# Optimization experiments

Hardware: AMD Instinct MI355X
Metric: run time of the kernel (lower is better)

The kernel has to match this reference:

```python
import jax, jax.numpy as jnp
import numpy as np

HEAD_DIM = 16

def setup_inputs() -> dict:
    key = jax.random.key(0)
    ks = jax.random.split(key, 9)
    dim = 256
    B, H, W = 8, 32, 32
    x  = jax.random.normal(ks[0], (B, H, W, dim), jnp.float32)
    # Conv2d weights in OIHW layout (torch convention), small init
    w3 = jax.random.normal(ks[1], (dim, dim, 1, 1), jnp.float32) * 0.05
    b3 = jax.random.normal(ks[2], (dim,), jnp.float32) * 0.01
    w5 = jax.random.normal(ks[3], (dim, dim, 3, 3), jnp.float32) * 0.02
    b5 = jax.random.normal(ks[4], (dim,), jnp.float32) * 0.01
    w7 = jax.random.normal(ks[5], (dim, dim, 5, 5), jnp.float32) * 0.01
    b7 = jax.random.normal(ks[6], (dim,), jnp.float32) * 0.01
    # nn.Linear weight: (out_features=dim, in_features=attention_dim=dim), no bias
    wp = jax.random.normal(ks[7], (dim, dim), jnp.float32) * 0.05
    return {"x": x, "w3": w3, "b3": b3, "w5": w5, "b5": b5, "w7": w7, "b7": b7, "wp": wp}

def _conv2d_same(x_nchw, w_oihw, b):
    y = jax.lax.conv_general_dilated(
        x_nchw, w_oihw, window_strides=(1, 1), padding='SAME',
        dimension_numbers=('NCHW', 'OIHW', 'NCHW'))
    return y + b[None, :, None, None]

def reference(x, w3, b3, w5, b5, w7, b7, wp):
    B, H, W, C = x.shape
    N = H * W
    nh = C // HEAD_DIM            # num_heads
    scale = HEAD_DIM ** (-0.5)
    xc = jnp.transpose(x, (0, 3, 1, 2))  # NCHW
    # q: 1x1 conv, v: 3x3 conv, k: 5x5 conv (names match the torch code)
    q = _conv2d_same(xc, w3, b3).reshape(B, nh, N, HEAD_DIM)
    v = _conv2d_same(xc, w5, b5).reshape(B, nh, N, HEAD_DIM)
    k = _conv2d_same(xc, w7, b7).reshape(B, nh, N, HEAD_DIM)
    attn = jax.nn.softmax(jnp.einsum('bhnd,bhmd->bhnm', q, k) * scale, axis=-1)
    out = jnp.einsum('bhnm,bhmd->bhnd', attn, v)        # [B, nh, N, hd]
    out = jnp.transpose(out, (0, 2, 1, 3)).reshape(B, H, W, nh * HEAD_DIM)
    return out @ wp.T                                   # Linear, no bias
```

## Files before the change

### kernel.cpp

```cpp
#include <hip/hip_runtime.h>
#include <hip/hip_bf16.h>

#define DIM 256
#define HW  1024

typedef __attribute__((ext_vector_type(8))) short short8;
typedef __attribute__((ext_vector_type(4))) float floatx4;
typedef __attribute__((ext_vector_type(16))) float floatx16;
typedef __attribute__((address_space(1))) const unsigned int g_u32;
typedef __attribute__((address_space(3))) unsigned int l_u32;

#define QSCALE 0.36067376022224085f

__device__ inline unsigned short f2bf(float f) {
  union { float f; unsigned u; } v;
  v.f = f;
  unsigned u = v.u;
  u += 0x7fffu + ((u >> 16) & 1u);
  return (unsigned short)(u >> 16);
}

__global__ void detect_kernel(const unsigned short* __restrict__ xr,
                              int* __restrict__ flag) {
  __shared__ int cnt;
  if (threadIdx.x == 0) cnt = 0;
  __syncthreads();
  int local = 0;
  for (int i = threadIdx.x; i < 8192; i += 256) {
    unsigned short u = xr[i];
    if ((u & 0x7F80u) == 0x7F80u) local++;
  }
  if (local) atomicAdd(&cnt, local);
  __syncthreads();
  if (threadIdx.x == 0) *flag = (cnt > 0) ? 1 : 0;
}

__device__ inline float ldin(const void* p, long i, int isf32) {
  if (isf32) return ((const float*)p)[i];
  union { unsigned u; float f; } v;
  v.u = ((unsigned)((const unsigned short*)p)[i]) << 16;
  return v.f;
}

__device__ inline void frag_repack(const void* __restrict__ w,
                                   unsigned short* __restrict__ wF, int KK,
                                   int local_blk, int t, int isf32) {
  const int idx = local_blk * 256 + t;
  const int j    = idx & 7;
  const int lane = (idx >> 3) & 63;
  const int co16 = (idx >> 9) & 15;
  const int c8   = (idx >> 13) & 7;
  const int tap  = idx >> 16;
  const int co = (co16 << 4) | (lane & 15);
  const int ci = (c8 << 5) + ((lane >> 4) << 3) + j;
  wF[idx] = f2bf(ldin(w, (long)(co * 256 + ci) * KK + tap, isf32));
}

__global__ void prep_kernel(const void* __restrict__ x,
                            const void* __restrict__ w3,
                            const void* __restrict__ b3,
                            const void* __restrict__ w5,
                            const void* __restrict__ b5,
                            const void* __restrict__ w7,
                            const void* __restrict__ b7,
                            const void* __restrict__ wp,
                            unsigned short* __restrict__ xbf,
                            unsigned short* __restrict__ wF3,
                            unsigned short* __restrict__ wF5,
                            unsigned short* __restrict__ wF7,
                            unsigned short* __restrict__ wpF,
                            float* __restrict__ bc,
                            const int* __restrict__ flag) {
  const int isf32 = *flag;
  const int bid = blockIdx.x;
  const int t = threadIdx.x;
  if (bid < 2048) {
    const int i = (bid * 256 + t) * 4;
    if (isf32) {
      const float4 v = *(const float4*)((const float*)x + i);
      ushort4 o;
      o.x = f2bf(v.x); o.y = f2bf(v.y); o.z = f2bf(v.z); o.w = f2bf(v.w);
      *(ushort4*)(xbf + i) = o;
    } else {
      *(ushort4*)(xbf + i) = *(const ushort4*)((const unsigned short*)x + i);
    }
  } else if (bid < 2304) {
    frag_repack(w3, wF3, 1, bid - 2048, t, isf32);
  } else if (bid < 4608) {
    frag_repack(w5, wF5, 9, bid - 2304, t, isf32);
  } else if (bid < 11008) {
    frag_repack(w7, wF7, 25, bid - 4608, t, isf32);
  } else if (bid < 11264) {
    frag_repack(wp, wpF, 1, bid - 11008, t, isf32);
  } else {
#pragma unroll
    for (int r = 0; r < 3; ++r) {
      const int i = r * 256 + t;
      const void* src = (i < 256) ? b3 : (i < 512) ? b5 : b7;
      bc[i] = ldin(src, i & 255, isf32);
    }
  }
}

__global__ __launch_bounds__(256, 2) void convqkv_kernel(
    const unsigned short* __restrict__ xbf,
    const unsigned short* __restrict__ wFq,
    const unsigned short* __restrict__ wFv,
    const unsigned short* __restrict__ wFk,
    const float* __restrict__ bc,
    unsigned short* __restrict__ qOut,
    unsigned short* __restrict__ vOut,
    unsigned short* __restrict__ kOut) {
  constexpr int WC = 36;
  constexpr int CELLS = 12 * WC;
  constexpr int LOADS = CELLS * 4;
  __shared__ unsigned short Xs[CELLS * 40];
  __shared__ unsigned short Bs[36 * 512];
  const int t    = threadIdx.x;
  const int bid  = blockIdx.x;
  const int cog0 = bid & 15;
  const int co0  = cog0 << 4;
  const int m0   = (bid >> 4) << 8;
  const int b    = m0 >> 10;
  const int n0   = m0 & 1023;
  const int r0   = n0 >> 5;
  const int wv   = t >> 6;
  const int lane = t & 63;
  const int l15  = lane & 15;
  const int quad = lane >> 4;

  floatx4 aq[4] = {}, av[4] = {}, ak[4] = {};

  for (int c8 = 0; c8 < 8; ++c8) {
    uint4 xreg[7];
#pragma unroll
    for (int rr = 0; rr < 7; ++rr) {
      const int id = rr * 256 + t;
      const int cell = id >> 2, part = id & 3;
      const int hr = cell / WC, wc = cell - hr * WC;
      const int xr = r0 + hr - 2, xc = wc - 2;
      const bool ok = (id < LOADS) && ((unsigned)xr < 32u) &&
                      ((unsigned)xc < 32u);
      const int cr = xr < 0 ? 0 : (xr > 31 ? 31 : xr);
      const int cc = xc < 0 ? 0 : (xc > 31 ? 31 : xc);
      uint4 v = *(const uint4*)&xbf[(((b * 32 + cr) * 32 + cc) << 8) +
                                    (c8 << 5) + (part << 3)];
      if (!ok) v = make_uint4(0, 0, 0, 0);
      xreg[rr] = v;
    }
    __syncthreads();
#pragma unroll
    for (int rr = 0; rr < 9; ++rr) {
      const int tap = (rr << 2) + wv;
      if (tap < 35) {
        const unsigned short* src;
        if (tap < 25) {
          src = &wFk[((((tap << 3) + c8) << 4) + cog0) * 512];
        } else if (tap < 34) {
          src = &wFv[(((((tap - 25) << 3) + c8) << 4) + cog0) * 512];
        } else {
          src = &wFq[((c8 << 4) + cog0) * 512];
        }
        __builtin_amdgcn_global_load_lds((g_u32*)(src + (lane << 3)),
                                         (l_u32*)&Bs[tap << 9], 16, 0, 0);
      }
    }
#pragma unroll
    for (int rr = 0; rr < 7; ++rr) {
      const int id = rr * 256 + t;
      if (id < LOADS)
        *(uint4*)&Xs[(id >> 2) * 40 + ((id & 3) << 3)] = xreg[rr];
    }
    __syncthreads();

#pragma unroll
    for (int tap = 0; tap < 25; ++tap) {
      const int kh = tap / 5, kw = tap % 5;
      const bool vv = (kh >= 1 && kh <= 3 && kw >= 1 && kw <= 3);
      short8 a[4];
#pragma unroll
      for (int rr2 = 0; rr2 < 2; ++rr2) {
#pragma unroll
        for (int ch = 0; ch < 2; ++ch) {
          const unsigned short* xs =
              &Xs[(((wv << 1) + rr2 + kh) * WC + (ch << 4) + l15 + kw) * 40 +
                  (quad << 3)];
          a[(rr2 << 1) + ch] = *(const short8*)xs;
        }
      }
      const short8 kb = *(const short8*)&Bs[(tap << 9) + (lane << 3)];
#pragma unroll
      for (int f = 0; f < 4; ++f)
        ak[f] = __builtin_amdgcn_mfma_f32_16x16x32_bf16(a[f], kb, ak[f],
                                                        0, 0, 0);
      if (vv) {
        const int vt = (kh - 1) * 3 + (kw - 1);
        const short8 vb = *(const short8*)&Bs[((25 + vt) << 9) + (lane << 3)];
#pragma unroll
        for (int f = 0; f < 4; ++f)
          av[f] = __builtin_amdgcn_mfma_f32_16x16x32_bf16(a[f], vb, av[f],
                                                          0, 0, 0);
      }
      if (tap == 12) {
        const short8 qb = *(const short8*)&Bs[(34 << 9) + (lane << 3)];
#pragma unroll
        for (int f = 0; f < 4; ++f)
          aq[f] = __builtin_amdgcn_mfma_f32_16x16x32_bf16(a[f], qb, aq[f],
                                                          0, 0, 0);
      }
    }
  }
#pragma unroll
  for (int rr2 = 0; rr2 < 2; ++rr2) {
#pragma unroll
    for (int ch = 0; ch < 2; ++ch) {
      const int f = (rr2 << 1) + ch;
      const int co = co0 + l15;
      const int slab = (b << 4) + (co >> 4);
      const int clo = co & 15;
      const int nb = n0 + (wv << 6) + (rr2 << 5) + (ch << 4) + (quad << 2);
      {
        const float bj = bc[co];
        floatx4 a = aq[f];
        ushort4 pk4;
        pk4.x = f2bf((a[0] + bj) * QSCALE);
        pk4.y = f2bf((a[1] + bj) * QSCALE);
        pk4.z = f2bf((a[2] + bj) * QSCALE);
        pk4.w = f2bf((a[3] + bj) * QSCALE);
        *(ushort4*)&qOut[(slab << 14) + (clo << 10) + nb] = pk4;
      }
      {
        const float bj = bc[512 + co];
        floatx4 a = ak[f];
        ushort4 pk4;
        pk4.x = f2bf(a[0] + bj); pk4.y = f2bf(a[1] + bj);
        pk4.z = f2bf(a[2] + bj); pk4.w = f2bf(a[3] + bj);
        *(ushort4*)&kOut[(slab << 14) + (clo << 10) + nb] = pk4;
      }
      {
        const float bj = bc[256 + co];
        floatx4 a = av[f];
        const int base = (slab << 14) + (clo << 6);
#pragma unroll
        for (int i = 0; i < 4; ++i) {
          const int n = nb + i;
          vOut[base + ((n & 15) << 10) + (n >> 4)] = f2bf(a[i] + bj);
        }
      }
    }
  }
}

__global__ __launch_bounds__(256, 4) void attn_mfma_kernel(
    const unsigned short* __restrict__ qg,
    const unsigned short* __restrict__ kg,
    const unsigned short* __restrict__ vg,
    unsigned short* __restrict__ out2) {
  __shared__ __align__(16) unsigned short Pb[4][32][40];
  const int t    = threadIdx.x;
  const int w    = t >> 6;
  const int lane = t & 63;
  const int slab = blockIdx.x >> 3;
  const int rb   = blockIdx.x & 7;
  const int b = slab >> 4;
  const int h = slab & 15;
  const int l31  = lane & 31;
  const int hl   = lane >> 5;
  const int l15  = lane & 15;
  const int quad = lane >> 4;

  const unsigned short* Kb = kg + (slab << 14);
  const unsigned short* Vb = vg + (slab << 14);

  const int row0 = (rb << 7) + (w << 5);
  const short8 qa =
      *(const short8*)&qg[(slab << 14) + ((row0 + l31) << 4) + (hl << 3)];

  const short onebf = (short)0x3F80;
  const short8 ones = {onebf, onebf, onebf, onebf, onebf, onebf, onebf, onebf};

  floatx4 acco[2] = {}, asum[2] = {};

  for (int kc = 0; kc < 1024; kc += 32) {
    const short8 kb = *(const short8*)&Kb[((kc + l31) << 4) + (hl << 3)];
    floatx16 s = {};
    s = __builtin_amdgcn_mfma_f32_32x32x16_bf16(qa, kb, s, 0, 0, 0);
#pragma unroll
    for (int r = 0; r < 16; ++r) {
      const float e = exp2f(s[r]);
      const int row = (r & 3) + ((r >> 2) << 3) + (hl << 2);
      Pb[w][row][l31] = f2bf(e);
    }
    const short8 vb = *(const short8*)&Vb[(l15 << 10) + kc + (quad << 3)];
#pragma unroll
    for (int tt = 0; tt < 2; ++tt) {
      const short8 pa = *(const short8*)&Pb[w][(tt << 4) + l15][quad << 3];
      acco[tt] =
          __builtin_amdgcn_mfma_f32_16x16x32_bf16(pa, vb, acco[tt], 0, 0, 0);
      asum[tt] =
          __builtin_amdgcn_mfma_f32_16x16x32_bf16(pa, ones, asum[tt], 0, 0, 0);
    }
  }
#pragma unroll
  for (int tt = 0; tt < 2; ++tt) {
#pragma unroll
    for (int r = 0; r < 4; ++r) {
      const int nloc = (tt << 4) + (quad << 2) + r;
      const float val = acco[tt][r] / asum[tt][r];
      const int n = row0 + nloc;
      out2[(((b << 10) + n) << 8) + (h << 4) + l15] = f2bf(val);
    }
  }
}

__global__ __launch_bounds__(256) void linear_mfma_kernel(
    const unsigned short* __restrict__ inp,
    const unsigned short* __restrict__ wpF,
    void* __restrict__ out, const int* __restrict__ flag) {
  __shared__ unsigned short As[64 * 40];
  const int isf32 = *flag;
  const int t   = threadIdx.x;
  const int m0  = blockIdx.x << 6;
  const int co0 = blockIdx.y << 6;
  const int wv   = t >> 6;
  const int lane = t & 63;
  const int wm = (wv & 1) << 5;
  const int wn = (wv >> 1) << 5;
  const int l15  = lane & 15;
  const int quad = lane >> 4;
  const int cogb = (co0 >> 4) + (wn >> 4);
  const int rowS = t >> 2;
  const int partS = t & 3;

  floatx4 acc[2][2] = {};

  short8 cb0, cb1;
  {
    const unsigned short* wptr = &wpF[(cogb << 9) + (lane << 3)];
    cb0 = *(const short8*)wptr;
    cb1 = *(const short8*)(wptr + 512);
  }
  for (int c8 = 0; c8 < 8; ++c8) {
    const uint4 v = *(const uint4*)&inp[((m0 + rowS) << 8) + (c8 << 5) +
                                        (partS << 3)];
    short8 nb0 = {}, nb1 = {};
    if (c8 + 1 < 8) {
      const unsigned short* wptr =
          &wpF[((((c8 + 1) << 4) + cogb) << 9) + (lane << 3)];
      nb0 = *(const short8*)wptr;
      nb1 = *(const short8*)(wptr + 512);
    }
    __syncthreads();
    *(uint4*)&As[rowS * 40 + (partS << 3)] = v;
    __syncthreads();
    const unsigned short* xs = &As[(wm + l15) * 40 + (quad << 3)];
    const short8 afr0 = *(const short8*)xs;
    const short8 afr1 = *(const short8*)(xs + 16 * 40);
    acc[0][0] = __builtin_amdgcn_mfma_f32_16x16x32_bf16(afr0, cb0,
                                                        acc[0][0], 0, 0, 0);
    acc[0][1] = __builtin_amdgcn_mfma_f32_16x16x32_bf16(afr0, cb1,
                                                        acc[0][1], 0, 0, 0);
    acc[1][0] = __builtin_amdgcn_mfma_f32_16x16x32_bf16(afr1, cb0,
                                                        acc[1][0], 0, 0, 0);
    acc[1][1] = __builtin_amdgcn_mfma_f32_16x16x32_bf16(afr1, cb1,
                                                        acc[1][1], 0, 0, 0);
    cb0 = nb0; cb1 = nb1;
  }
#pragma unroll
  for (int mi = 0; mi < 2; ++mi) {
#pragma unroll
    for (int ni = 0; ni < 2; ++ni) {
      const int co = co0 + wn + (ni << 4) + l15;
      const int mb = m0 + wm + (mi << 4) + (quad << 2);
      floatx4 a = acc[mi][ni];
      if (!isf32) {
        unsigned short* o16 = (unsigned short*)out;
#pragma unroll
        for (int r = 0; r < 4; ++r) o16[(mb + r) * 256 + co] = f2bf(a[r]);
      } else {
        float* o32 = (float*)out;
#pragma unroll
        for (int r = 0; r < 4; ++r) o32[(mb + r) * 256 + co] = a[r];
      }
    }
  }
}

extern "C" void kernel_launch(void* const* d_in, const int* in_sizes, int n_in,
                              void* d_out, int out_size, void* d_ws,
                              size_t ws_size, hipStream_t stream) {
  const void* x  = d_in[0];
  const void* w3 = d_in[1];
  const void* b3 = d_in[2];
  const void* w5 = d_in[3];
  const void* b5 = d_in[4];
  const void* w7 = d_in[5];
  const void* b7 = d_in[6];
  const void* wp = d_in[7];

  char* p = (char*)d_ws;
  int* flag = (int*)p;                       p += 256;
  unsigned short* xbf = (unsigned short*)p;  p += 4u * 1024 * 1024;
  unsigned short* wF3 = (unsigned short*)p;  p += 131072;
  unsigned short* wF5 = (unsigned short*)p;  p += 1179648;
  unsigned short* wF7 = (unsigned short*)p;  p += 3276800;
  unsigned short* wpF = (unsigned short*)p;  p += 131072;
  float* bc = (float*)p;                     p += 4096;
  unsigned short* qc  = (unsigned short*)p;  p += 4194304;
  unsigned short* kT  = (unsigned short*)p;  p += 4194304;
  unsigned short* vT  = (unsigned short*)p;  p += 4194304;
  unsigned short* o2b = (unsigned short*)p;  p += 4194304;

  detect_kernel<<<1, 256, 0, stream>>>((const unsigned short*)x, flag);

  prep_kernel<<<11265, 256, 0, stream>>>(x, w3, b3, w5, b5, w7, b7, wp, xbf,
                                         wF3, wF5, wF7, wpF, bc, flag);

  convqkv_kernel<<<512, 256, 0, stream>>>(xbf, wF3, wF5, wF7, bc, qc, vT, kT);

  attn_mfma_kernel<<<1024, 256, 0, stream>>>(qc, kT, vT, o2b);

  dim3 lg(128, 4);
  linear_mfma_kernel<<<lg, 256, 0, stream>>>(o2b, wpF, d_out, flag);
}
```

Baseline: 181.2 us.

## Split prep into x-convert and LDS-staged weight repack; use fast exp2 and truncation

Measured after the change: 179.5 us. No clear change (-1.0%).

```diff
diff --git a/kernel.cpp b/kernel.cpp
--- a/kernel.cpp
+++ b/kernel.cpp
@@ -18,6 +18,12 @@
   unsigned u = v.u;
   u += 0x7fffu + ((u >> 16) & 1u);
   return (unsigned short)(u >> 16);
+}
+
+__device__ inline unsigned short f2bf_trunc(float f) {
+  union { float f; unsigned u; } v;
+  v.f = f;
+  return (unsigned short)(v.u >> 16);
 }
 
 __global__ void detect_kernel(const unsigned short* __restrict__ xr,
@@ -42,56 +48,65 @@
   return v.f;
 }
 
-__device__ inline void frag_repack(const void* __restrict__ w,
-                                   unsigned short* __restrict__ wF, int KK,
-                                   int local_blk, int t, int isf32) {
-  const int idx = local_blk * 256 + t;
-  const int j    = idx & 7;
-  const int lane = (idx >> 3) & 63;
-  const int co16 = (idx >> 9) & 15;
-  const int c8   = (idx >> 13) & 7;
-  const int tap  = idx >> 16;
-  const int co = (co16 << 4) | (lane & 15);
-  const int ci = (c8 << 5) + ((lane >> 4) << 3) + j;
-  wF[idx] = f2bf(ldin(w, (long)(co * 256 + ci) * KK + tap, isf32));
-}
-
-__global__ void prep_kernel(const void* __restrict__ x,
-                            const void* __restrict__ w3,
-                            const void* __restrict__ b3,
-                            const void* __restrict__ w5,
-                            const void* __restrict__ b5,
-                            const void* __restrict__ w7,
-                            const void* __restrict__ b7,
-                            const void* __restrict__ wp,
-                            unsigned short* __restrict__ xbf,
-                            unsigned short* __restrict__ wF3,
-                            unsigned short* __restrict__ wF5,
-                            unsigned short* __restrict__ wF7,
-                            unsigned short* __restrict__ wpF,
-                            float* __restrict__ bc,
-                            const int* __restrict__ flag) {
+__global__ __launch_bounds__(256) void xconv_kernel(
+    const void* __restrict__ x, unsigned short* __restrict__ xbf,
+    const int* __restrict__ flag) {
+  const int isf32 = *flag;
+  const int i = (blockIdx.x * 256 + threadIdx.x) * 4;
+  if (isf32) {
+    const float4 v = *(const float4*)((const float*)x + i);
+    ushort4 o;
+    o.x = f2bf(v.x); o.y = f2bf(v.y); o.z = f2bf(v.z); o.w = f2bf(v.w);
+    *(ushort4*)(xbf + i) = o;
+  } else {
+    *(ushort4*)(xbf + i) = *(const ushort4*)((const unsigned short*)x + i);
+  }
+}
+
+__device__ inline void frag_repack2(const void* __restrict__ w,
+                                    unsigned short* __restrict__ wF, int KK,
+                                    int slice, float* __restrict__ Wl,
+                                    int isf32) {
+  const int t = threadIdx.x;
+  const int co16 = slice & 15;
+  const int c8   = slice >> 4;
+  const int RE = 32 * KK;
+  for (int r = 0; r < 16; ++r) {
+    const long base = ((long)((co16 * 16 + r) * 256 + c8 * 32)) * KK;
+    for (int i = t; i < RE; i += 256) Wl[r * RE + i] = ldin(w, base + i, isf32);
+  }
+  __syncthreads();
+  for (int tap = 0; tap < KK; ++tap) {
+    unsigned short* dst = wF + ((((tap << 3) + c8) << 4) + co16) * 512;
+    for (int i = t; i < 512; i += 256) {
+      const int lane = i >> 3, j = i & 7;
+      const int col = lane & 15;
+      const int cis = ((lane >> 4) << 3) + j;
+      dst[i] = f2bf(Wl[(col * 32 + cis) * KK + tap]);
+    }
+  }
+}
+
+__global__ __launch_bounds__(256) void wrepack_kernel(
+    const void* __restrict__ w3, const void* __restrict__ b3,
+    const void* __restrict__ w5, const void* __restrict__ b5,
+    const void* __restrict__ w7, const void* __restrict__ b7,
+    const void* __restrict__ wp,
+    unsigned short* __restrict__ wF3, unsigned short* __restrict__ wF5,
+    unsigned short* __restrict__ wF7, unsigned short* __restrict__ wpF,
+    float* __restrict__ bc, const int* __restrict__ flag) {
+  __shared__ float Wl[12800];
   const int isf32 = *flag;
   const int bid = blockIdx.x;
   const int t = threadIdx.x;
-  if (bid < 2048) {
-    const int i = (bid * 256 + t) * 4;
-    if (isf32) {
-      const float4 v = *(const float4*)((const float*)x + i);
-      ushort4 o;
-      o.x = f2bf(v.x); o.y = f2bf(v.y); o.z = f2bf(v.z); o.w = f2bf(v.w);
-      *(ushort4*)(xbf + i) = o;
-    } else {
-      *(ushort4*)(xbf + i) = *(const ushort4*)((const unsigned short*)x + i);
-    }
-  } else if (bid < 2304) {
-    frag_repack(w3, wF3, 1, bid - 2048, t, isf32);
-  } else if (bid < 4608) {
-    frag_repack(w5, wF5, 9, bid - 2304, t, isf32);
-  } else if (bid < 11008) {
-    frag_repack(w7, wF7, 25, bid - 4608, t, isf32);
-  } else if (bid < 11264) {
-    frag_repack(wp, wpF, 1, bid - 11008, t, isf32);
+  if (bid < 128) {
+    frag_repack2(w7, wF7, 25, bid, Wl, isf32);
+  } else if (bid < 256) {
+    frag_repack2(w5, wF5, 9, bid - 128, Wl, isf32);
+  } else if (bid < 384) {
+    frag_repack2(w3, wF3, 1, bid - 256, Wl, isf32);
+  } else if (bid < 512) {
+    frag_repack2(wp, wpF, 1, bid - 384, Wl, isf32);
   } else {
 #pragma unroll
     for (int r = 0; r < 3; ++r) {
@@ -287,9 +302,9 @@
     s = __builtin_amdgcn_mfma_f32_32x32x16_bf16(qa, kb, s, 0, 0, 0);
 #pragma unroll
     for (int r = 0; r < 16; ++r) {
-      const float e = exp2f(s[r]);
+      const float e = __builtin_amdgcn_exp2f(s[r]);
       const int row = (r & 3) + ((r >> 2) << 3) + (hl << 2);
-      Pb[w][row][l31] = f2bf(e);
+      Pb[w][row][l31] = f2bf_trunc(e);
     }
     const short8 vb = *(const short8*)&Vb[(l15 << 10) + kc + (quad << 3)];
 #pragma unroll
@@ -413,8 +428,9 @@
 
   detect_kernel<<<1, 256, 0, stream>>>((const unsigned short*)x, flag);
 
-  prep_kernel<<<11265, 256, 0, stream>>>(x, w3, b3, w5, b5, w7, b7, wp, xbf,
-                                         wF3, wF5, wF7, wpF, bc, flag);
+  xconv_kernel<<<2048, 256, 0, stream>>>(x, xbf, flag);
+  wrepack_kernel<<<513, 256, 0, stream>>>(w3, b3, w5, b5, w7, b7, wp, wF3,
+                                          wF5, wF7, wpF, bc, flag);
 
   convqkv_kernel<<<512, 256, 0, stream>>>(xbf, wF3, wF5, wF7, bc, qc, vT, kT);
 
```
